# Kernel tuning notes

Hardware: AMD Instinct MI355X
Metric: run time of the kernel (lower is better)

Reference implementation:

```python
import jax, jax.numpy as jnp
import numpy as np

XYZ_MIN = -1.0
XYZ_MAX = 1.0
MULTIRES = 4  # viewdirs positional-embedding frequencies


def trilerp(grid, pts):
    """Trilinear interpolation, align_corners=True, border clamp.
    grid: [C, X, Y, Z]; pts: [N, 3] in world coords. Returns [N, C]."""
    res = np.array(grid.shape[1:])  # (X, Y, Z)
    resf = jnp.asarray(res, dtype=pts.dtype)
    u = (pts - XYZ_MIN) / (XYZ_MAX - XYZ_MIN) * (resf - 1.0)  # [N,3] voxel coords
    u = jnp.clip(u, 0.0, resf - 1.0)
    i0 = jnp.clip(jnp.floor(u).astype(jnp.int32), 0, jnp.asarray(res - 2, dtype=jnp.int32))
    f = u - i0.astype(pts.dtype)  # [N,3] fractional offsets
    out = 0.0
    for dx in (0, 1):
        wx = f[:, 0] if dx else 1.0 - f[:, 0]
        for dy in (0, 1):
            wy = f[:, 1] if dy else 1.0 - f[:, 1]
            for dz in (0, 1):
                wz = f[:, 2] if dz else 1.0 - f[:, 2]
                g = grid[:, i0[:, 0] + dx, i0[:, 1] + dy, i0[:, 2] + dz]  # [C,N]
                out = out + (wx * wy * wz) * g
    return out.T  # [N,C]


def embed_viewdirs(v):
    """NeRF positional embedding: [v, sin(2^k v), cos(2^k v)] -> [N, 3+3*2*MULTIRES]."""
    freqs = 2.0 ** jnp.arange(MULTIRES, dtype=v.dtype)  # [F]
    ang = v[:, None, :] * freqs[None, :, None]  # [N,F,3]
    n = v.shape[0]
    return jnp.concatenate([v, jnp.sin(ang).reshape(n, -1), jnp.cos(ang).reshape(n, -1)], axis=-1)


def setup_inputs() -> dict:
    key = jax.random.key(0)
    ks = jax.random.split(key, 8)
    n = 2097152
    pts = jax.random.uniform(ks[0], (n, 3), jnp.float32, minval=XYZ_MIN, maxval=XYZ_MAX)
    vd = jax.random.normal(ks[1], (n, 3), jnp.float32)
    viewdirs = vd / jnp.linalg.norm(vd, axis=-1, keepdims=True)
    density_grid = jax.random.normal(ks[2], (1, 160, 160, 160), jnp.float32)
    color_grid = jax.random.normal(ks[3], (12, 160, 160, 160), jnp.float32)
    in_dim = 9 + 3 + 3 * 2 * MULTIRES  # k0_view (12-3) + viewdirs embed (27) = 36
    w0 = jax.random.normal(ks[4], (in_dim, 128), jnp.float32) * (1.0 / np.sqrt(in_dim))
    w1 = jax.random.normal(ks[5], (128, 128), jnp.float32) * (1.0 / np.sqrt(128))
    w2 = jax.random.normal(ks[6], (128, 3), jnp.float32) * (1.0 / np.sqrt(128))
    return {
        "pts": pts, "viewdirs": viewdirs,
        "density_grid": density_grid, "color_grid": color_grid,
        "w0": w0, "b0": jnp.zeros((128,), jnp.float32),
        "w1": w1, "b1": jnp.zeros((128,), jnp.float32),
        "w2": w2, "b2": jnp.zeros((3,), jnp.float32),
    }


def reference(pts, viewdirs, density_grid, color_grid, w0, b0, w1, b1, w2, b2):
    # density branch (use_densitynet=False -> raw interpolated density, channels=1)
    pts_density = trilerp(density_grid, pts)  # [N,1]
    # color branch with color_emission: k0 = [diffuse(3), view-dep(9)]
    k0 = trilerp(color_grid, pts)  # [N,12]
    k0_diffuse, k0_view = k0[:, :3], k0[:, 3:]
    feat = jnp.concatenate([k0_view, embed_viewdirs(viewdirs)], axis=-1)  # [N,36]
    h = jax.nn.relu(feat @ w0 + b0)
    h = jax.nn.relu(h @ w1 + b1)
    k0_logit = h @ w2 + b2  # [N,3]
    pts_color = jax.nn.sigmoid(k0_logit + k0_diffuse)
    return jnp.concatenate([pts_color, pts_density], axis=-1)  # [N,4]
```

## Files before the change

### kernel.cpp

```cpp
#include <hip/hip_runtime.h>
#include <hip/hip_bf16.h>
#include <math.h>

#define RES   160
#define RES2  (160*160)
#define RES3  (160*160*160)
#define TG_ELEMS ((size_t)RES3 * 16)
#define TG_BYTES (TG_ELEMS * 2)

#define BLOB_BYTES  47104
#define BLOB_SHORTS 22528
#define BLOB_FLOATS 512
#define A1_OFF      12288
#define B1P_OFF     45056
#define W2P_OFF     45568

typedef __attribute__((ext_vector_type(8)))  short s16x8;
typedef __attribute__((ext_vector_type(2)))  float f32x2;
typedef __attribute__((ext_vector_type(4)))  float f32x4;
typedef __attribute__((ext_vector_type(16))) float f32x16;
typedef __attribute__((ext_vector_type(4)))  int   i32x4;

__device__ __forceinline__ unsigned short f2bf(float x) {
    union { float f; unsigned u; } v; v.f = x;
    unsigned r = v.u + 0x7FFFu + ((v.u >> 16) & 1u);
    return (unsigned short)(r >> 16);
}
__device__ __forceinline__ unsigned cvtpk(float lo, float hi) {
    unsigned r;
    asm("v_cvt_pk_bf16_f32 %0, %1, %2" : "=v"(r) : "v"(lo), "v"(hi));
    return r;
}
__device__ __forceinline__ float bf_lo(unsigned u) {
    union { unsigned u; float f; } v; v.u = u << 16; return v.f;
}
__device__ __forceinline__ float bf_hi(unsigned u) {
    union { unsigned u; float f; } v; v.u = u & 0xFFFF0000u; return v.f;
}
__device__ __forceinline__ unsigned cvtpk_relu(float a, float b) {
    return cvtpk(fmaxf(a, 0.0f), fmaxf(b, 0.0f));
}
__device__ __forceinline__ void plswap(unsigned &a, unsigned &b) {
    asm("v_permlane32_swap_b32 %0, %1" : "+v"(a), "+v"(b));
}
__device__ __forceinline__ float sum_halves(float x) {
    unsigned a = __float_as_uint(x), b = a;
    plswap(a, b);
    return __uint_as_float(a) + __uint_as_float(b);
}
__device__ __forceinline__ f32x2 pkfma(f32x2 a, f32x2 b, f32x2 c) {
    f32x2 r;
    asm("v_pk_fma_f32 %0, %1, %2, %3" : "=v"(r) : "v"(a), "v"(b), "v"(c));
    return r;
}
__device__ __forceinline__ f32x2 pkmul(f32x2 a, f32x2 b) {
    f32x2 r;
    asm("v_pk_mul_f32 %0, %1, %2" : "=v"(r) : "v"(a), "v"(b));
    return r;
}

__device__ __forceinline__ float blob_short_val(int i, const float* __restrict__ w0,
                                                const float* __restrict__ b0,
                                                const float* __restrict__ w1) {
    if (i < 6144) {
        int e = i & 7, s = i >> 3;
        int lo = s & 31, r = s >> 5;
        int hi = r & 1, t = r >> 1;
        int wm = t / 3, ks = t - wm * 3;
        int k = ks * 16 + hi * 8 + e, n = wm * 32 + lo;
        return k < 36 ? w0[k * 128 + n] : (k == 36 ? b0[n] : 0.0f);
    } else {
        int i2 = i - 6144;
        int e = i2 & 7, s = i2 >> 3;
        int lo = s & 31, r = s >> 5;
        int hi = r & 1, t = r >> 1;
        int wm = t >> 3, ks = t & 7;
        int k = ks * 16 + hi * 8 + e, n = wm * 32 + lo;
        return w1[k * 128 + n];
    }
}
__device__ __forceinline__ float blob_float_val(int j, const float* __restrict__ b1,
                                                const float* __restrict__ w2) {
    if (j < 128) {
        int c = j & 3, r = j >> 2, hi = r & 1, t = r >> 1;
        int g = t & 3, wm = t >> 2;
        return b1[wm * 32 + 8 * g + 4 * hi + c];
    } else {
        int j2 = j - 128;
        int c  = j2 & 3;
        int t  = j2 >> 2;
        int cc = t % 3;
        int u  = t / 3;
        int hi = u & 1, v = u >> 1;
        int g  = v & 3, wm = v >> 2;
        return w2[(wm * 32 + 8 * g + 4 * hi + c) * 3 + cc];
    }
}

__global__ __launch_bounds__(256) void make_tg(
    const float* __restrict__ dgrid, const float* __restrict__ cgrid,
    short* __restrict__ tg)
{
    const int v = blockIdx.x * 256 + threadIdx.x;
    float vals[13];
    #pragma unroll
    for (int c = 0; c < 12; ++c) vals[c] = cgrid[(size_t)c * RES3 + v];
    vals[12] = dgrid[v];

    i32x4 r0 = { (int)cvtpk(vals[0], vals[1]),  (int)cvtpk(vals[2],  vals[3]),
                 (int)cvtpk(vals[4], vals[5]),  (int)cvtpk(vals[6],  vals[7]) };
    i32x4 r1 = { (int)cvtpk(vals[8], vals[9]),  (int)cvtpk(vals[10], vals[11]),
                 (int)cvtpk(vals[12], 0.0f),    0 };
    *(i32x4*)&tg[(size_t)v * 16 + 0] = r0;
    *(i32x4*)&tg[(size_t)v * 16 + 8] = r1;
}

__global__ __launch_bounds__(256) void prepack(
    const float* __restrict__ w0, const float* __restrict__ b0,
    const float* __restrict__ w1, const float* __restrict__ b1,
    const float* __restrict__ w2, char* __restrict__ blob)
{
    int t = blockIdx.x * 256 + threadIdx.x;
    if (t < BLOB_SHORTS) {
        ((short*)blob)[t] = (short)f2bf(blob_short_val(t, w0, b0, w1));
    } else if (t < BLOB_SHORTS + BLOB_FLOATS) {
        int j = t - BLOB_SHORTS;
        ((float*)(blob + B1P_OFF))[j] = blob_float_val(j, b1, w2);
    }
}

template<bool TG, bool PRE>
__global__ __launch_bounds__(512, 4) void dvgo_fused(
    const float* __restrict__ pts, const float* __restrict__ vdirs,
    const float* __restrict__ dgrid, const float* __restrict__ cgrid,
    const short* __restrict__ tg, const char* __restrict__ blob,
    const float* __restrict__ w0, const float* __restrict__ b0,
    const float* __restrict__ w1, const float* __restrict__ b1,
    const float* __restrict__ w2, const float* __restrict__ b2,
    float* __restrict__ out)
{
    __shared__ __align__(16) char smem[BLOB_BYTES];
    const int tid  = threadIdx.x;
    const int lane = tid & 63;
    const int wv   = tid >> 6;
    const int lo   = lane & 31;
    const int hi   = lane >> 5;

    if (PRE) {
        const i32x4* src = (const i32x4*)blob;
        i32x4* dst = (i32x4*)smem;
        for (int i = tid; i < BLOB_BYTES / 16; i += 512) dst[i] = src[i];
    } else {
        for (int i = tid; i < BLOB_SHORTS; i += 512)
            ((short*)smem)[i] = (short)f2bf(blob_short_val(i, w0, b0, w1));
        for (int i = tid; i < BLOB_FLOATS; i += 512)
            ((float*)(smem + B1P_OFF))[i] = blob_float_val(i, b1, w2);
    }

    const int p = blockIdx.x * 512 + tid;
    float P0 = pts[p*3+0], P1 = pts[p*3+1], P2 = pts[p*3+2];
    float V0 = vdirs[p*3+0], V1 = vdirs[p*3+1], V2 = vdirs[p*3+2];

    int   ii[3];
    float ff[3];
    float Pv[3] = {P0, P1, P2};
    #pragma unroll
    for (int d = 0; d < 3; ++d) {
        float u = (Pv[d] + 1.0f) * 79.5f;
        u = fminf(fmaxf(u, 0.0f), 159.0f);
        int i0 = (int)u;
        if (i0 > 158) i0 = 158;
        ii[d] = i0;
        ff[d] = u - (float)i0;
    }
    const float fx = ff[0], fy = ff[1], fz = ff[2];
    const float wxy0 = (1.0f-fx)*(1.0f-fy);
    const float wxy1 = (1.0f-fx)*fy;
    const float wxy2 = fx*(1.0f-fy);
    const float wxy3 = fx*fy;

    float dens;
    float col[12];

    if (TG) {
        const int base16 = ((ii[0]*RES + ii[1])*RES + ii[2]) * 16;
        const short* q00 = tg + base16;
        const short* q01 = q00 + RES*16;
        const short* q10 = q00 + RES2*16;
        const short* q11 = q10 + RES*16;

        f32x2 cv[7];
        #pragma unroll
        for (int pr = 0; pr < 7; ++pr) cv[pr] = f32x2{0.0f, 0.0f};

        const f32x2 fzv   = { fz, fz };
        const f32x2 omfzv = { 1.0f - fz, 1.0f - fz };

        const short* qs[4] = { q00, q01, q10, q11 };
        const float  wsx[4] = { wxy0, wxy1, wxy2, wxy3 };
        #pragma unroll
        for (int cn = 0; cn < 4; ++cn) {
            const short* q = qs[cn];
            i32x4 u0 = *(const i32x4*)(q);
            i32x4 u1v = *(const i32x4*)(q + 8);
            i32x4 u2 = *(const i32x4*)(q + 16);
            i32x4 u3 = *(const i32x4*)(q + 24);
            unsigned av[8] = { (unsigned)u0[0], (unsigned)u0[1], (unsigned)u0[2], (unsigned)u0[3],
                               (unsigned)u1v[0], (unsigned)u1v[1], (unsigned)u1v[2], (unsigned)u1v[3] };
            unsigned bv[8] = { (unsigned)u2[0], (unsigned)u2[1], (unsigned)u2[2], (unsigned)u2[3],
                               (unsigned)u3[0], (unsigned)u3[1], (unsigned)u3[2], (unsigned)u3[3] };
            const f32x2 wv2 = { wsx[cn], wsx[cn] };
            #pragma unroll
            for (int pr = 0; pr < 7; ++pr) {
                f32x2 va = { bf_lo(av[pr]), bf_hi(av[pr]) };
                f32x2 vb = { bf_lo(bv[pr]), bf_hi(bv[pr]) };
                f32x2 lz = pkfma(fzv, vb, pkmul(omfzv, va));
                cv[pr] = pkfma(wv2, lz, cv[pr]);
            }
        }
        #pragma unroll
        for (int c = 0; c < 12; ++c) col[c] = (c & 1) ? cv[c >> 1].y : cv[c >> 1].x;
        dens = cv[6].x;
    } else {
        const int base = (ii[0]*RES + ii[1])*RES + ii[2];
        const int o0 = base, o1 = base + RES, o2 = base + RES2, o3 = base + RES2 + RES;
        auto tl = [&](const float* __restrict__ g) -> float {
            float a0 = g[o0], a1 = g[o0+1];
            float c0 = g[o1], c1 = g[o1+1];
            float d0 = g[o2], d1 = g[o2+1];
            float e0 = g[o3], e1 = g[o3+1];
            float v0 = a0 + fz*(a1-a0);
            float v1 = c0 + fz*(c1-c0);
            float v2 = d0 + fz*(d1-d0);
            float v3 = e0 + fz*(e1-e0);
            return wxy0*v0 + wxy1*v1 + wxy2*v2 + wxy3*v3;
        };
        dens = tl(dgrid);
        #pragma unroll
        for (int c = 0; c < 12; ++c) col[c] = tl(cgrid + (size_t)c * RES3);
    }

    float ft[36];
    #pragma unroll
    for (int j = 0; j < 9; ++j) ft[j] = col[3+j];
    ft[9] = V0; ft[10] = V1; ft[11] = V2;
    float Vv[3] = {V0, V1, V2};
    #pragma unroll
    for (int d = 0; d < 3; ++d) {
        float s1, c1;
        __sincosf(Vv[d], &s1, &c1);
        float s2 = 2.0f*s1*c1,  c2 = __builtin_fmaf(-2.0f*s1, s1, 1.0f);
        float s4 = 2.0f*s2*c2,  c4 = __builtin_fmaf(-2.0f*s2, s2, 1.0f);
        float s8 = 2.0f*s4*c4,  c8 = __builtin_fmaf(-2.0f*s4, s4, 1.0f);
        ft[12 + d] = s1; ft[15 + d] = s2; ft[18 + d] = s4; ft[21 + d] = s8;
        ft[24 + d] = c1; ft[27 + d] = c2; ft[30 + d] = c4; ft[33 + d] = c8;
    }
    unsigned fpk[24];
    #pragma unroll
    for (int j = 0; j < 18; ++j) fpk[j] = cvtpk(ft[2*j], ft[2*j+1]);
    fpk[18] = cvtpk(1.0f, 0.0f);
    #pragma unroll
    for (int j = 19; j < 24; ++j) fpk[j] = 0u;

    #pragma unroll
    for (int ks = 0; ks < 3; ++ks)
        #pragma unroll
        for (int d = 0; d < 4; ++d)
            plswap(fpk[ks*8 + d], fpk[ks*8 + 4 + d]);

    const float col0v = col[0], col1v = col[1], col2v = col[2];
    const float scol0 = __shfl_xor(col0v, 32, 64);
    const float scol1 = __shfl_xor(col1v, 32, 64);
    const float scol2 = __shfl_xor(col2v, 32, 64);
    const float sdens = __shfl_xor(dens,  32, 64);
    const float b2v0 = b2[0], b2v1 = b2[1], b2v2 = b2[2];

    __syncthreads();

    const char*  a0p  = smem + lane * 16;
    const char*  a1p  = smem + A1_OFF + lane * 16;
    const float* b1ph = (const float*)(smem + B1P_OFF) + hi * 4;
    const float* w2ph = (const float*)(smem + W2P_OFF) + hi * 12;

    #pragma unroll
    for (int pt = 0; pt < 2; ++pt) {
        f32x16 acc0[4];
        #pragma unroll
        for (int w = 0; w < 4; ++w)
            #pragma unroll
            for (int r = 0; r < 16; ++r) acc0[w][r] = 0.0f;

        #pragma unroll
        for (int ks = 0; ks < 3; ++ks) {
            i32x4 bi = { (int)fpk[ks*8 + 4*pt + 0], (int)fpk[ks*8 + 4*pt + 1],
                         (int)fpk[ks*8 + 4*pt + 2], (int)fpk[ks*8 + 4*pt + 3] };
            s16x8 B = __builtin_bit_cast(s16x8, bi);
            #pragma unroll
            for (int w = 0; w < 4; ++w) {
                s16x8 A = *(const s16x8*)(a0p + (w*3 + ks) * 1024);
                acc0[w] = __builtin_amdgcn_mfma_f32_32x32x16_bf16(A, B, acc0[w], 0, 0, 0);
            }
        }

        unsigned u1[4][8];
        #pragma unroll
        for (int w = 0; w < 4; ++w)
            #pragma unroll
            for (int g = 0; g < 4; ++g) {
                u1[w][2*g+0] = cvtpk_relu(acc0[w][4*g+0], acc0[w][4*g+1]);
                u1[w][2*g+1] = cvtpk_relu(acc0[w][4*g+2], acc0[w][4*g+3]);
            }

        f32x16 acc1[4];
        #pragma unroll
        for (int w = 0; w < 4; ++w)
            #pragma unroll
            for (int g = 0; g < 4; ++g) {
                f32x4 bv = *(const f32x4*)(b1ph + (w*4 + g) * 8);
                acc1[w][4*g+0] = bv[0]; acc1[w][4*g+1] = bv[1];
                acc1[w][4*g+2] = bv[2]; acc1[w][4*g+3] = bv[3];
            }
        #pragma unroll
        for (int ks = 0; ks < 8; ++ks) {
            const int w = ks >> 1, q = 4 * (ks & 1);
            plswap(u1[w][q+0], u1[w][q+2]);
            plswap(u1[w][q+1], u1[w][q+3]);
            i32x4 bi = { (int)u1[w][q+0], (int)u1[w][q+1],
                         (int)u1[w][q+2], (int)u1[w][q+3] };
            s16x8 B = __builtin_bit_cast(s16x8, bi);
            #pragma unroll
            for (int wm = 0; wm < 4; ++wm) {
                s16x8 A = *(const s16x8*)(a1p + (wm*8 + ks) * 1024);
                acc1[wm] = __builtin_amdgcn_mfma_f32_32x32x16_bf16(A, B, acc1[wm], 0, 0, 0);
            }
        }

        f32x2 pa0 = {0.0f, 0.0f}, pa1 = {0.0f, 0.0f}, pa2 = {0.0f, 0.0f};
        #pragma unroll
        for (int w = 0; w < 4; ++w)
            #pragma unroll
            for (int g = 0; g < 4; ++g) {
                const float* wrow = w2ph + (w*4 + g) * 24;
                f32x4 q0 = *(const f32x4*)(wrow + 0);
                f32x4 q1 = *(const f32x4*)(wrow + 4);
                f32x4 q2 = *(const f32x4*)(wrow + 8);
                f32x2 v01 = { fmaxf(acc1[w][4*g+0], 0.0f), fmaxf(acc1[w][4*g+1], 0.0f) };
                f32x2 v23 = { fmaxf(acc1[w][4*g+2], 0.0f), fmaxf(acc1[w][4*g+3], 0.0f) };
                pa0 = pkfma(v01, f32x2{q0[0], q0[1]}, pa0);
                pa0 = pkfma(v23, f32x2{q0[2], q0[3]}, pa0);
                pa1 = pkfma(v01, f32x2{q1[0], q1[1]}, pa1);
                pa1 = pkfma(v23, f32x2{q1[2], q1[3]}, pa1);
                pa2 = pkfma(v01, f32x2{q2[0], q2[1]}, pa2);
                pa2 = pkfma(v23, f32x2{q2[2], q2[3]}, pa2);
            }
        float p0 = sum_halves(pa0.x + pa0.y);
        float p1 = sum_halves(pa1.x + pa1.y);
        float p2 = sum_halves(pa2.x + pa2.y);

        const float d0 = pt ? scol0 : col0v;
        const float d1 = pt ? scol1 : col1v;
        const float d2 = pt ? scol2 : col2v;
        const float dn = pt ? sdens : dens;
        if (hi == 0) {
            float x0 = p0 + b2v0 + d0;
            float x1 = p1 + b2v1 + d1;
            float x2 = p2 + b2v2 + d2;
            f32x4 o = { 1.0f / (1.0f + __expf(-x0)),
                        1.0f / (1.0f + __expf(-x1)),
                        1.0f / (1.0f + __expf(-x2)),
                        dn };
            const int gp = blockIdx.x * 512 + wv * 64 + pt * 32 + lo;
            *(f32x4*)(out + (size_t)gp * 4) = o;
        }
    }
}

extern "C" void kernel_launch(void* const* d_in, const int* in_sizes, int n_in,
                              void* d_out, int out_size, void* d_ws, size_t ws_size,
                              hipStream_t stream) {
    const float* pts = (const float*)d_in[0];
    const float* vd  = (const float*)d_in[1];
    const float* dg  = (const float*)d_in[2];
    const float* cg  = (const float*)d_in[3];
    const float* w0  = (const float*)d_in[4];
    const float* b0  = (const float*)d_in[5];
    const float* w1  = (const float*)d_in[6];
    const float* b1  = (const float*)d_in[7];
    const float* w2  = (const float*)d_in[8];
    const float* b2  = (const float*)d_in[9];
    float* out = (float*)d_out;

    const int n = in_sizes[0] / 3;
    const int blocks = n / 512;

    if (ws_size >= TG_BYTES + BLOB_BYTES) {
        short* tg = (short*)d_ws;
        char* blob = (char*)d_ws + TG_BYTES;
        make_tg<<<RES3/256, 256, 0, stream>>>(dg, cg, tg);
        prepack<<<(BLOB_SHORTS + BLOB_FLOATS + 255)/256, 256, 0, stream>>>(
            w0, b0, w1, b1, w2, blob);
        dvgo_fused<true, true><<<blocks, 512, 0, stream>>>(
            pts, vd, dg, cg, tg, blob, w0, b0, w1, b1, w2, b2, out);
    } else if (ws_size >= TG_BYTES) {
        short* tg = (short*)d_ws;
        make_tg<<<RES3/256, 256, 0, stream>>>(dg, cg, tg);
        dvgo_fused<true, false><<<blocks, 512, 0, stream>>>(
            pts, vd, dg, cg, tg, nullptr, w0, b0, w1, b1, w2, b2, out);
    } else {
        dvgo_fused<false, false><<<blocks, 512, 0, stream>>>(
            pts, vd, dg, cg, nullptr, nullptr, w0, b0, w1, b1, w2, b2, out);
    }
}
```

Measured before the change: 272.4 us.

## Pack color grid as fp8 y/z-neighbor quads with separate bf16 density pairs

Adds a preprocessing kernel that stores, for each voxel, its four (y,z) neighbor corners in one 64-byte record. View-dependent channels are encoded as fp8 and diffuse channels as bf16, and density goes into a separate bf16 z-pair array. The main kernel then fetches two contiguous 64-byte records plus four 4-byte density words per point, instead of four 64-byte corner records. The aim is fewer scattered gathers in the trilinear lookup. In exchange it quantizes nine color channels to fp8 and writes a 262 MB packed grid each call, which raises prepass write traffic and risks accuracy.

```diff
diff --git a/kernel.cpp b/kernel.cpp
--- a/kernel.cpp
+++ b/kernel.cpp
@@ -7,6 +7,9 @@
 #define RES3  (160*160*160)
 #define TG_ELEMS ((size_t)RES3 * 16)
 #define TG_BYTES (TG_ELEMS * 2)
+
+#define QG_BYTES  ((size_t)RES3 * 64)
+#define DGP_BYTES ((size_t)RES3 * 4)
 
 #define BLOB_BYTES  47104
 #define BLOB_SHORTS 22528
@@ -57,6 +60,69 @@
     f32x2 r;
     asm("v_pk_mul_f32 %0, %1, %2" : "=v"(r) : "v"(a), "v"(b));
     return r;
+}
+
+__device__ __forceinline__ unsigned enc8_manual(float x) {
+    unsigned u = __float_as_uint(x);
+    unsigned s = (u >> 24) & 0x80u;
+    unsigned mag = u & 0x7FFFFFFFu;
+    if (mag < 0x3C800000u) return s;
+    if (mag >= 0x43E00000u) return s | 0x7Eu;
+    unsigned r = mag + 0x7FFFFu + ((mag >> 20) & 1u);
+    return s | ((r >> 20) - 960u);
+}
+__device__ __forceinline__ float dec8_manual(unsigned b) {
+    unsigned s = (b & 0x80u) << 24;
+    unsigned em = b & 0x7Fu;
+    if (em == 0) return __uint_as_float(s);
+    if (em < 8) {
+        float v = (float)em * 0.001953125f;
+        return (b & 0x80u) ? -v : v;
+    }
+    return __uint_as_float(s | ((em + 960u) << 20));
+}
+template<bool HI>
+__device__ __forceinline__ unsigned pk_enc8(float a, float b, unsigned old) {
+#if __has_builtin(__builtin_amdgcn_cvt_pk_fp8_f32)
+    return (unsigned)__builtin_amdgcn_cvt_pk_fp8_f32(a, b, (int)old, HI);
+#else
+    unsigned w = enc8_manual(a) | (enc8_manual(b) << 8);
+    return HI ? ((old & 0xFFFFu) | (w << 16)) : ((old & 0xFFFF0000u) | w);
+#endif
+}
+template<bool HI>
+__device__ __forceinline__ f32x2 pk_dec8(unsigned w) {
+#if __has_builtin(__builtin_amdgcn_cvt_pk_f32_fp8)
+    return __builtin_amdgcn_cvt_pk_f32_fp8((int)w, HI);
+#else
+    unsigned h = HI ? (w >> 16) : (w & 0xFFFFu);
+    return f32x2{ dec8_manual(h & 0xFFu), dec8_manual((h >> 8) & 0xFFu) };
+#endif
+}
+
+__device__ __forceinline__ f32x2 plerp(f32x2 a, f32x2 b, float t) {
+    f32x2 tv = { t, t };
+    f32x2 d  = { b.x - a.x, b.y - a.y };
+    return pkfma(tv, d, a);
+}
+__device__ __forceinline__ float slerp(float a, float b, float t) {
+    return __builtin_fmaf(t, b - a, a);
+}
+
+template<int W, bool HI>
+__device__ __forceinline__ f32x2 qlerp(const i32x4 (&A)[4], const i32x4 (&B)[4],
+                                       float fx, float fy, float fz) {
+    f32x2 a00 = pk_dec8<HI>((unsigned)A[0][W]);
+    f32x2 a01 = pk_dec8<HI>((unsigned)A[1][W]);
+    f32x2 a10 = pk_dec8<HI>((unsigned)A[2][W]);
+    f32x2 a11 = pk_dec8<HI>((unsigned)A[3][W]);
+    f32x2 b00 = pk_dec8<HI>((unsigned)B[0][W]);
+    f32x2 b01 = pk_dec8<HI>((unsigned)B[1][W]);
+    f32x2 b10 = pk_dec8<HI>((unsigned)B[2][W]);
+    f32x2 b11 = pk_dec8<HI>((unsigned)B[3][W]);
+    f32x2 ya = plerp(plerp(a00, a01, fz), plerp(a10, a11, fz), fy);
+    f32x2 yb = plerp(plerp(b00, b01, fz), plerp(b10, b11, fz), fy);
+    return plerp(ya, yb, fx);
 }
 
 __device__ __forceinline__ float blob_short_val(int i, const float* __restrict__ w0,
@@ -115,6 +181,51 @@
     *(i32x4*)&tg[(size_t)v * 16 + 8] = r1;
 }
 
+__global__ __launch_bounds__(256) void make_pack(
+    const float* __restrict__ dgrid, const float* __restrict__ cgrid,
+    char* __restrict__ qg, unsigned* __restrict__ dgp)
+{
+    const int v = blockIdx.x * 256 + threadIdx.x;
+    const int z = v % RES;
+    const int xy = v / RES;
+    const int y = xy % RES;
+    const int x = xy / RES;
+    const int y1 = (y < RES-1) ? y + 1 : y;
+    const int z1 = (z < RES-1) ? z + 1 : z;
+
+    const int vz1 = (x * RES + y) * RES + z1;
+    dgp[v] = cvtpk(dgrid[v], dgrid[vz1]);
+
+    const int yy[2] = { y, y1 };
+    const int zz[2] = { z, z1 };
+    i32x4 outw[4];
+    #pragma unroll
+    for (int dy = 0; dy < 2; ++dy) {
+        #pragma unroll
+        for (int dz = 0; dz < 2; ++dz) {
+            const size_t base = (size_t)(x * RES + yy[dy]) * RES + zz[dz];
+            float vv[9];
+            #pragma unroll
+            for (int c = 0; c < 9; ++c) vv[c] = cgrid[(size_t)(3 + c) * RES3 + base];
+            float d0 = cgrid[(size_t)0 * RES3 + base];
+            float d1 = cgrid[(size_t)1 * RES3 + base];
+            float d2 = cgrid[(size_t)2 * RES3 + base];
+            unsigned w0 = pk_enc8<false>(vv[0], vv[1], 0u);
+            w0 = pk_enc8<true>(vv[2], vv[3], w0);
+            unsigned w1 = pk_enc8<false>(vv[4], vv[5], 0u);
+            w1 = pk_enc8<true>(vv[6], vv[7], w1);
+            unsigned w2 = pk_enc8<false>(vv[8], 0.0f, 0u);
+            w2 = (w2 & 0xFFFFu) | ((unsigned)f2bf(d0) << 16);
+            unsigned w3 = (unsigned)f2bf(d1) | ((unsigned)f2bf(d2) << 16);
+            outw[dy * 2 + dz] = i32x4{ (int)w0, (int)w1, (int)w2, (int)w3 };
+        }
+    }
+    char* dst = qg + (size_t)v * 64;
+    #pragma unroll
+    for (int s = 0; s < 4; ++s)
+        *(i32x4*)(dst + s * 16) = outw[s];
+}
+
 __global__ __launch_bounds__(256) void prepack(
     const float* __restrict__ w0, const float* __restrict__ b0,
     const float* __restrict__ w1, const float* __restrict__ b1,
@@ -129,11 +240,12 @@
     }
 }
 
-template<bool TG, bool PRE>
+template<int MODE, bool PRE>
 __global__ __launch_bounds__(512, 4) void dvgo_fused(
     const float* __restrict__ pts, const float* __restrict__ vdirs,
     const float* __restrict__ dgrid, const float* __restrict__ cgrid,
-    const short* __restrict__ tg, const char* __restrict__ blob,
+    const short* __restrict__ tg, const char* __restrict__ qg,
+    const unsigned* __restrict__ dgp, const char* __restrict__ blob,
     const float* __restrict__ w0, const float* __restrict__ b0,
     const float* __restrict__ w1, const float* __restrict__ b1,
     const float* __restrict__ w2, const float* __restrict__ b2,
@@ -174,15 +286,67 @@
         ff[d] = u - (float)i0;
     }
     const float fx = ff[0], fy = ff[1], fz = ff[2];
-    const float wxy0 = (1.0f-fx)*(1.0f-fy);
-    const float wxy1 = (1.0f-fx)*fy;
-    const float wxy2 = fx*(1.0f-fy);
-    const float wxy3 = fx*fy;
 
     float dens;
     float col[12];
 
-    if (TG) {
+    if (MODE == 2) {
+        const size_t vidx = (size_t)(ii[0] * RES + ii[1]) * RES + ii[2];
+        const char* qa = qg + vidx * 64;
+        const char* qb = qa + (size_t)RES2 * 64;
+        i32x4 A[4], B[4];
+        #pragma unroll
+        for (int s = 0; s < 4; ++s) A[s] = *(const i32x4*)(qa + s * 16);
+        #pragma unroll
+        for (int s = 0; s < 4; ++s) B[s] = *(const i32x4*)(qb + s * 16);
+
+        f32x2 r0 = qlerp<0, false>(A, B, fx, fy, fz);
+        f32x2 r1 = qlerp<0, true >(A, B, fx, fy, fz);
+        f32x2 r2 = qlerp<1, false>(A, B, fx, fy, fz);
+        f32x2 r3 = qlerp<1, true >(A, B, fx, fy, fz);
+        f32x2 r4 = qlerp<2, false>(A, B, fx, fy, fz);
+        col[3] = r0.x;  col[4]  = r0.y;
+        col[5] = r1.x;  col[6]  = r1.y;
+        col[7] = r2.x;  col[8]  = r2.y;
+        col[9] = r3.x;  col[10] = r3.y;
+        col[11] = r4.x;
+
+        {
+            f32x2 a00 = { bf_hi((unsigned)A[0][2]), bf_lo((unsigned)A[0][3]) };
+            f32x2 a01 = { bf_hi((unsigned)A[1][2]), bf_lo((unsigned)A[1][3]) };
+            f32x2 a10 = { bf_hi((unsigned)A[2][2]), bf_lo((unsigned)A[2][3]) };
+            f32x2 a11 = { bf_hi((unsigned)A[3][2]), bf_lo((unsigned)A[3][3]) };
+            f32x2 b00 = { bf_hi((unsigned)B[0][2]), bf_lo((unsigned)B[0][3]) };
+            f32x2 b01 = { bf_hi((unsigned)B[1][2]), bf_lo((unsigned)B[1][3]) };
+            f32x2 b10 = { bf_hi((unsigned)B[2][2]), bf_lo((unsigned)B[2][3]) };
+            f32x2 b11 = { bf_hi((unsigned)B[3][2]), bf_lo((unsigned)B[3][3]) };
+            f32x2 r = plerp(plerp(plerp(a00, a01, fz), plerp(a10, a11, fz), fy),
+                            plerp(plerp(b00, b01, fz), plerp(b10, b11, fz), fy), fx);
+            col[0] = r.x; col[1] = r.y;
+            float c00 = bf_hi((unsigned)A[0][3]), c01 = bf_hi((unsigned)A[1][3]);
+            float c10 = bf_hi((unsigned)A[2][3]), c11 = bf_hi((unsigned)A[3][3]);
+            float e00 = bf_hi((unsigned)B[0][3]), e01 = bf_hi((unsigned)B[1][3]);
+            float e10 = bf_hi((unsigned)B[2][3]), e11 = bf_hi((unsigned)B[3][3]);
+            col[2] = slerp(slerp(slerp(c00, c01, fz), slerp(c10, c11, fz), fy),
+                           slerp(slerp(e00, e01, fz), slerp(e10, e11, fz), fy), fx);
+        }
+        {
+            const size_t i00 = (size_t)(ii[0] * RES + ii[1]) * RES + ii[2];
+            unsigned da0 = dgp[i00];
+            unsigned da1 = dgp[i00 + RES];
+            unsigned db0 = dgp[i00 + RES2];
+            unsigned db1 = dgp[i00 + RES2 + RES];
+            float za0 = slerp(bf_lo(da0), bf_hi(da0), fz);
+            float za1 = slerp(bf_lo(da1), bf_hi(da1), fz);
+            float zb0 = slerp(bf_lo(db0), bf_hi(db0), fz);
+            float zb1 = slerp(bf_lo(db1), bf_hi(db1), fz);
+            dens = slerp(slerp(za0, za1, fy), slerp(zb0, zb1, fy), fx);
+        }
+    } else if (MODE == 1) {
+        const float wxy0 = (1.0f-fx)*(1.0f-fy);
+        const float wxy1 = (1.0f-fx)*fy;
+        const float wxy2 = fx*(1.0f-fy);
+        const float wxy3 = fx*fy;
         const int base16 = ((ii[0]*RES + ii[1])*RES + ii[2]) * 16;
         const short* q00 = tg + base16;
         const short* q01 = q00 + RES*16;
@@ -192,10 +356,8 @@
         f32x2 cv[7];
         #pragma unroll
         for (int pr = 0; pr < 7; ++pr) cv[pr] = f32x2{0.0f, 0.0f};
-
         const f32x2 fzv   = { fz, fz };
         const f32x2 omfzv = { 1.0f - fz, 1.0f - fz };
-
         const short* qs[4] = { q00, q01, q10, q11 };
         const float  wsx[4] = { wxy0, wxy1, wxy2, wxy3 };
         #pragma unroll
@@ -222,6 +384,10 @@
         for (int c = 0; c < 12; ++c) col[c] = (c & 1) ? cv[c >> 1].y : cv[c >> 1].x;
         dens = cv[6].x;
     } else {
+        const float wxy0 = (1.0f-fx)*(1.0f-fy);
+        const float wxy1 = (1.0f-fx)*fy;
+        const float wxy2 = fx*(1.0f-fy);
+        const float wxy3 = fx*fy;
         const int base = (ii[0]*RES + ii[1])*RES + ii[2];
         const int o0 = base, o1 = base + RES, o2 = base + RES2, o3 = base + RES2 + RES;
         auto tl = [&](const float* __restrict__ g) -> float {
@@ -393,21 +559,30 @@
     const int n = in_sizes[0] / 3;
     const int blocks = n / 512;
 
-    if (ws_size >= TG_BYTES + BLOB_BYTES) {
+    if (ws_size >= QG_BYTES + DGP_BYTES + BLOB_BYTES) {
+        char* qg = (char*)d_ws;
+        unsigned* dgp = (unsigned*)((char*)d_ws + QG_BYTES);
+        char* blob = (char*)d_ws + QG_BYTES + DGP_BYTES;
+        make_pack<<<RES3/256, 256, 0, stream>>>(dg, cg, qg, dgp);
+        prepack<<<(BLOB_SHORTS + BLOB_FLOATS + 255)/256, 256, 0, stream>>>(
+            w0, b0, w1, b1, w2, blob);
+        dvgo_fused<2, true><<<blocks, 512, 0, stream>>>(
+            pts, vd, dg, cg, nullptr, qg, dgp, blob, w0, b0, w1, b1, w2, b2, out);
+    } else if (ws_size >= TG_BYTES + BLOB_BYTES) {
         short* tg = (short*)d_ws;
         char* blob = (char*)d_ws + TG_BYTES;
         make_tg<<<RES3/256, 256, 0, stream>>>(dg, cg, tg);
         prepack<<<(BLOB_SHORTS + BLOB_FLOATS + 255)/256, 256, 0, stream>>>(
             w0, b0, w1, b1, w2, blob);
-        dvgo_fused<true, true><<<blocks, 512, 0, stream>>>(
-            pts, vd, dg, cg, tg, blob, w0, b0, w1, b1, w2, b2, out);
+        dvgo_fused<1, true><<<blocks, 512, 0, stream>>>(
+            pts, vd, dg, cg, tg, nullptr, nullptr, blob, w0, b0, w1, b1, w2, b2, out);
     } else if (ws_size >= TG_BYTES) {
         short* tg = (short*)d_ws;
         make_tg<<<RES3/256, 256, 0, stream>>>(dg, cg, tg);
-        dvgo_fused<true, false><<<blocks, 512, 0, stream>>>(
-            pts, vd, dg, cg, tg, nullptr, w0, b0, w1, b1, w2, b2, out);
+        dvgo_fused<1, false><<<blocks, 512, 0, stream>>>(
+            pts, vd, dg, cg, tg, nullptr, nullptr, nullptr, w0, b0, w1, b1, w2, b2, out);
     } else {
-        dvgo_fused<false, false><<<blocks, 512, 0, stream>>>(
-            pts, vd, dg, cg, nullptr, nullptr, w0, b0, w1, b1, w2, b2, out);
-    }
-}
+        dvgo_fused<0, false><<<blocks, 512, 0, stream>>>(
+            pts, vd, dg, cg, nullptr, nullptr, nullptr, nullptr, w0, b0, w1, b1, w2, b2, out);
+    }
+}
```

New measurement: 367.8 us. +35.0%, slower.
